# Kernel tuning notes

Hardware: AMD Instinct MI355X
Metric: run time of the kernel (lower is better)

## Reference

```python
import jax, jax.numpy as jnp
import numpy as np

ALPHA = 1.0
BETA = 0.25

B, C, D = 65536, 1024, 64


def setup_inputs() -> dict:
    key = jax.random.key(0)
    k1, k2 = jax.random.split(key)
    z = jax.random.normal(k1, (B, D), dtype=jnp.float32)
    # xavier_normal init for the (C, D) codebook
    std = float(np.sqrt(2.0 / (C + D)))
    codebook = jax.random.normal(k2, (C, D), dtype=jnp.float32) * std
    return {"z": z, "codebook": codebook}


def reference(z, codebook):
    # pairwise squared distances d[b,c] = ||z_b - e_c||^2 via expanded norms
    zn2 = jnp.sum(z * z, axis=1, keepdims=True)          # [B,1]
    wn2 = jnp.sum(codebook * codebook, axis=1)            # [C]
    d = zn2 + wn2 - 2.0 * (z @ codebook.T)               # [B,C]
    # Student-t soft assignment (same value as torch's explicit diff-sum)
    q = jnp.power(1.0 / (1.0 + d / ALPHA), (ALPHA + 1.0) / 2.0)
    q = q / jnp.sum(q, axis=1, keepdims=True)
    # hard assignment: torch code uses argmax over d (faithful to source)
    idx = jnp.argmax(d, axis=1)                          # [B]
    # gather codebook rows (equals one-hot @ codebook)
    z_q = codebook[idx]                                  # [B,D]
    sg = jax.lax.stop_gradient
    loss = BETA * jnp.mean((sg(z_q) - z) ** 2) + jnp.mean((z_q - sg(z)) ** 2)
    # straight-through estimator
    z_q_st = z + sg(z_q - z)
    return q, z_q_st, loss
```

## Files before the change

### kernel.cpp

```cpp
#include <hip/hip_runtime.h>
#include <stdint.h>

#define NB    65536
#define NC    1024
#define ND    64
#define BR    32
#define NW    4


__global__ void vq_prep(const float* __restrict__ cb, float* __restrict__ ws) {
    int c = blockIdx.x * 64 + threadIdx.x;
    float s = 0.f;
    #pragma unroll 8
    for (int k = 0; k < ND; ++k) {
        float v = cb[c * ND + k];
        ws[2048 + k * NC + c] = v;
        s = fmaf(v, v, s);
    }
    ws[64 + c] = s;
}

__device__ inline unsigned long long shfl_xor_u64(unsigned long long v, int m) {
    unsigned lo = (unsigned)v, hi = (unsigned)(v >> 32);
    lo = __shfl_xor(lo, m, 64);
    hi = __shfl_xor(hi, m, 64);
    return ((unsigned long long)hi << 32) | (unsigned long long)lo;
}

__global__ __launch_bounds__(256, 2) void vq_main(
    const float* __restrict__ z, const float* __restrict__ cb,
    const float* __restrict__ ws, float* __restrict__ q_out,
    float* __restrict__ zq_out, float* __restrict__ loss_acc)
{
    const int rb = blockIdx.x * BR;
    const int L  = threadIdx.x;
    const float* __restrict__ zb = z + (size_t)rb * ND;
    const float4* __restrict__ cbT4 = (const float4*)(ws + 2048);
    const float4* __restrict__ wn24 = (const float4*)(ws + 64);

    __shared__ float part[256];
    __shared__ float zn2s[BR];
    __shared__ float sred[NW * BR];
    __shared__ unsigned long long kred[NW * BR];

    {
        const float4* z4 = (const float4*)zb;
        float4 a = z4[L * 2 + 0];
        float4 b = z4[L * 2 + 1];
        part[L] = a.x*a.x + a.y*a.y + a.z*a.z + a.w*a.w
                + b.x*b.x + b.y*b.y + b.z*b.z + b.w*b.w;
    }
    __syncthreads();
    if (L < BR) {
        float s = 0.f;
        #pragma unroll
        for (int j = 0; j < 8; ++j) s += part[L * 8 + j];
        zn2s[L] = s;
    }
    __syncthreads();

    float4 acc[BR];
    #pragma unroll
    for (int r = 0; r < BR; ++r) acc[r] = make_float4(0.f, 0.f, 0.f, 0.f);

    for (int kk = 0; kk < ND; kk += 4) {
        float4 c0 = cbT4[(size_t)(kk + 0) * 256 + L];
        float4 c1 = cbT4[(size_t)(kk + 1) * 256 + L];
        float4 c2 = cbT4[(size_t)(kk + 2) * 256 + L];
        float4 c3 = cbT4[(size_t)(kk + 3) * 256 + L];
        #pragma unroll
        for (int r = 0; r < BR; ++r) {
            float z0 = zb[r * ND + kk + 0];
            float z1 = zb[r * ND + kk + 1];
            float z2 = zb[r * ND + kk + 2];
            float z3 = zb[r * ND + kk + 3];
            float4 a = acc[r];
            a.x = fmaf(z0, c0.x, a.x); a.y = fmaf(z0, c0.y, a.y);
            a.z = fmaf(z0, c0.z, a.z); a.w = fmaf(z0, c0.w, a.w);
            a.x = fmaf(z1, c1.x, a.x); a.y = fmaf(z1, c1.y, a.y);
            a.z = fmaf(z1, c1.z, a.z); a.w = fmaf(z1, c1.w, a.w);
            a.x = fmaf(z2, c2.x, a.x); a.y = fmaf(z2, c2.y, a.y);
            a.z = fmaf(z2, c2.z, a.z); a.w = fmaf(z2, c2.w, a.w);
            a.x = fmaf(z3, c3.x, a.x); a.y = fmaf(z3, c3.y, a.y);
            a.z = fmaf(z3, c3.z, a.z); a.w = fmaf(z3, c3.w, a.w);
            acc[r] = a;
        }
    }

    const int wv = L >> 6, lane = L & 63;
    float4 w4 = wn24[L];
    const int c0i = 4 * L;

    #pragma unroll
    for (int r = 0; r < BR; ++r) {
        float zn2r = zn2s[r];
        float4 a = acc[r];
        float d0 = (zn2r + w4.x) - 2.f * a.x;
        float d1 = (zn2r + w4.y) - 2.f * a.y;
        float d2 = (zn2r + w4.z) - 2.f * a.z;
        float d3 = (zn2r + w4.w) - 2.f * a.w;
        float q0 = __builtin_amdgcn_rcpf(1.f + d0);
        float q1 = __builtin_amdgcn_rcpf(1.f + d1);
        float q2 = __builtin_amdgcn_rcpf(1.f + d2);
        float q3 = __builtin_amdgcn_rcpf(1.f + d3);
        acc[r] = make_float4(q0, q1, q2, q3);
        float ps = ((q0 + q1) + q2) + q3;
        unsigned long long k0 = ((unsigned long long)__float_as_uint(d0) << 32) | (unsigned)(1023 - (c0i + 0));
        unsigned long long k1 = ((unsigned long long)__float_as_uint(d1) << 32) | (unsigned)(1023 - (c0i + 1));
        unsigned long long k2 = ((unsigned long long)__float_as_uint(d2) << 32) | (unsigned)(1023 - (c0i + 2));
        unsigned long long k3 = ((unsigned long long)__float_as_uint(d3) << 32) | (unsigned)(1023 - (c0i + 3));
        unsigned long long ka = k0 > k1 ? k0 : k1;
        unsigned long long kb = k2 > k3 ? k2 : k3;
        unsigned long long key = ka > kb ? ka : kb;
        #pragma unroll
        for (int m = 1; m < 64; m <<= 1) {
            ps += __shfl_xor(ps, m, 64);
            unsigned long long ok = shfl_xor_u64(key, m);
            key = key > ok ? key : ok;
        }
        if (lane == 0) { sred[wv * BR + r] = ps; kred[wv * BR + r] = key; }
    }
    __syncthreads();

    #pragma unroll
    for (int r = 0; r < BR; ++r) {
        float fs = ((sred[0 * BR + r] + sred[1 * BR + r]) + sred[2 * BR + r]) + sred[3 * BR + r];
        float inv = __builtin_amdgcn_rcpf(fs);
        float4 a = acc[r];
        float4 o = make_float4(a.x * inv, a.y * inv, a.z * inv, a.w * inv);
        ((float4*)q_out)[(size_t)(rb + r) * (NC / 4) + L] = o;
    }

    float lsum = 0.f;
    #pragma unroll
    for (int i = 0; i < BR / NW; ++i) {
        int r = wv * (BR / NW) + i;
        unsigned long long ka = kred[0 * BR + r] > kred[1 * BR + r] ? kred[0 * BR + r] : kred[1 * BR + r];
        unsigned long long kb = kred[2 * BR + r] > kred[3 * BR + r] ? kred[2 * BR + r] : kred[3 * BR + r];
        unsigned long long km = ka > kb ? ka : kb;
        int bc = 1023 - (int)(unsigned)(km & 0xffffffffULL);
        float cv = cb[(size_t)bc * ND + lane];
        float zv = z[(size_t)(rb + r) * ND + lane];
        float t = cv - zv;
        zq_out[(size_t)(rb + r) * ND + lane] = zv + t;
        lsum = fmaf(t, t, lsum);
    }
    #pragma unroll
    for (int m = 1; m < 64; m <<= 1) lsum += __shfl_xor(lsum, m, 64);
    if (lane == 0) atomicAdd(loss_acc, lsum);
}

__global__ void vq_fin(const float* __restrict__ ws, float* __restrict__ loss_out) {
    if (threadIdx.x == 0) {
        float m = ws[0] / (float)((size_t)NB * ND);
        loss_out[0] = 0.25f * m + m;
    }
}

extern "C" void kernel_launch(void* const* d_in, const int* in_sizes, int n_in,
                              void* d_out, int out_size, void* d_ws, size_t ws_size,
                              hipStream_t stream) {
    const float* z  = (const float*)d_in[0];
    const float* cb = (const float*)d_in[1];
    float* q_out    = (float*)d_out;
    float* zq_out   = q_out + (size_t)NB * NC;
    float* loss_out = zq_out + (size_t)NB * ND;
    float* ws       = (float*)d_ws;

    hipMemsetAsync(d_ws, 0, 4, stream);
    vq_prep<<<NC / 64, 64, 0, stream>>>(cb, ws);
    vq_main<<<NB / BR, 256, 0, stream>>>(z, cb, ws, q_out, zq_out, ws);
    vq_fin<<<1, 64, 0, stream>>>(ws, loss_out);
}
```

Measured before the change: 419.9 us.

## Halve row tile, stage z rows in LDS, raise occupancy, vectorize prep

The main kernel now processes 16 rows per block instead of 32, stages the z tile in shared memory as float4 instead of reading scalar z values from global memory, and raises the launch-bound occupancy hint from 2 to 4 blocks per CU. The prep kernel is rewritten to use float4 loads with 16 threads per codebook row and a shuffle reduction for the norms. This aims to cut register pressure and improve latency hiding in the memory-bound q write phase. The trade-off is that each codebook column load is reused across half as many rows, doubling codebook traffic from L2.

```diff
diff --git a/kernel.cpp b/kernel.cpp
--- a/kernel.cpp
+++ b/kernel.cpp
@@ -4,20 +4,23 @@
 #define NB    65536
 #define NC    1024
 #define ND    64
-#define BR    32
+#define BR    16
 #define NW    4
 
 
 __global__ void vq_prep(const float* __restrict__ cb, float* __restrict__ ws) {
-    int c = blockIdx.x * 64 + threadIdx.x;
-    float s = 0.f;
-    #pragma unroll 8
-    for (int k = 0; k < ND; ++k) {
-        float v = cb[c * ND + k];
-        ws[2048 + k * NC + c] = v;
-        s = fmaf(v, v, s);
-    }
-    ws[64 + c] = s;
+    int gid = blockIdx.x * 256 + threadIdx.x;
+    int c  = gid >> 4;
+    int kq = gid & 15;
+    float4 v = ((const float4*)cb)[gid];
+    ws[2048 + (4 * kq + 0) * NC + c] = v.x;
+    ws[2048 + (4 * kq + 1) * NC + c] = v.y;
+    ws[2048 + (4 * kq + 2) * NC + c] = v.z;
+    ws[2048 + (4 * kq + 3) * NC + c] = v.w;
+    float s = v.x * v.x + v.y * v.y + v.z * v.z + v.w * v.w;
+    #pragma unroll
+    for (int m = 1; m < 16; m <<= 1) s += __shfl_xor(s, m, 64);
+    if ((threadIdx.x & 15) == 0) ws[64 + c] = s;
 }
 
 __device__ inline unsigned long long shfl_xor_u64(unsigned long long v, int m) {
@@ -27,34 +30,32 @@
     return ((unsigned long long)hi << 32) | (unsigned long long)lo;
 }
 
-__global__ __launch_bounds__(256, 2) void vq_main(
+__global__ __launch_bounds__(256, 4) void vq_main(
     const float* __restrict__ z, const float* __restrict__ cb,
     const float* __restrict__ ws, float* __restrict__ q_out,
     float* __restrict__ zq_out, float* __restrict__ loss_acc)
 {
     const int rb = blockIdx.x * BR;
     const int L  = threadIdx.x;
-    const float* __restrict__ zb = z + (size_t)rb * ND;
     const float4* __restrict__ cbT4 = (const float4*)(ws + 2048);
     const float4* __restrict__ wn24 = (const float4*)(ws + 64);
 
+    __shared__ float4 zs4[BR * 16];
     __shared__ float part[256];
     __shared__ float zn2s[BR];
     __shared__ float sred[NW * BR];
     __shared__ unsigned long long kred[NW * BR];
 
     {
-        const float4* z4 = (const float4*)zb;
-        float4 a = z4[L * 2 + 0];
-        float4 b = z4[L * 2 + 1];
-        part[L] = a.x*a.x + a.y*a.y + a.z*a.z + a.w*a.w
-                + b.x*b.x + b.y*b.y + b.z*b.z + b.w*b.w;
+        float4 v = ((const float4*)z)[(size_t)rb * 16 + L];
+        zs4[L] = v;
+        part[L] = v.x * v.x + v.y * v.y + v.z * v.z + v.w * v.w;
     }
     __syncthreads();
     if (L < BR) {
         float s = 0.f;
         #pragma unroll
-        for (int j = 0; j < 8; ++j) s += part[L * 8 + j];
+        for (int j = 0; j < 16; ++j) s += part[L * 16 + j];
         zn2s[L] = s;
     }
     __syncthreads();
@@ -63,26 +64,24 @@
     #pragma unroll
     for (int r = 0; r < BR; ++r) acc[r] = make_float4(0.f, 0.f, 0.f, 0.f);
 
-    for (int kk = 0; kk < ND; kk += 4) {
-        float4 c0 = cbT4[(size_t)(kk + 0) * 256 + L];
-        float4 c1 = cbT4[(size_t)(kk + 1) * 256 + L];
-        float4 c2 = cbT4[(size_t)(kk + 2) * 256 + L];
-        float4 c3 = cbT4[(size_t)(kk + 3) * 256 + L];
+    #pragma unroll 2
+    for (int kk = 0; kk < 16; ++kk) {
+        float4 c0 = cbT4[(size_t)(4 * kk + 0) * 256 + L];
+        float4 c1 = cbT4[(size_t)(4 * kk + 1) * 256 + L];
+        float4 c2 = cbT4[(size_t)(4 * kk + 2) * 256 + L];
+        float4 c3 = cbT4[(size_t)(4 * kk + 3) * 256 + L];
         #pragma unroll
         for (int r = 0; r < BR; ++r) {
-            float z0 = zb[r * ND + kk + 0];
-            float z1 = zb[r * ND + kk + 1];
-            float z2 = zb[r * ND + kk + 2];
-            float z3 = zb[r * ND + kk + 3];
+            float4 zr = zs4[r * 16 + kk];
             float4 a = acc[r];
-            a.x = fmaf(z0, c0.x, a.x); a.y = fmaf(z0, c0.y, a.y);
-            a.z = fmaf(z0, c0.z, a.z); a.w = fmaf(z0, c0.w, a.w);
-            a.x = fmaf(z1, c1.x, a.x); a.y = fmaf(z1, c1.y, a.y);
-            a.z = fmaf(z1, c1.z, a.z); a.w = fmaf(z1, c1.w, a.w);
-            a.x = fmaf(z2, c2.x, a.x); a.y = fmaf(z2, c2.y, a.y);
-            a.z = fmaf(z2, c2.z, a.z); a.w = fmaf(z2, c2.w, a.w);
-            a.x = fmaf(z3, c3.x, a.x); a.y = fmaf(z3, c3.y, a.y);
-            a.z = fmaf(z3, c3.z, a.z); a.w = fmaf(z3, c3.w, a.w);
+            a.x = fmaf(zr.x, c0.x, a.x); a.y = fmaf(zr.x, c0.y, a.y);
+            a.z = fmaf(zr.x, c0.z, a.z); a.w = fmaf(zr.x, c0.w, a.w);
+            a.x = fmaf(zr.y, c1.x, a.x); a.y = fmaf(zr.y, c1.y, a.y);
+            a.z = fmaf(zr.y, c1.z, a.z); a.w = fmaf(zr.y, c1.w, a.w);
+            a.x = fmaf(zr.z, c2.x, a.x); a.y = fmaf(zr.z, c2.y, a.y);
+            a.z = fmaf(zr.z, c2.z, a.z); a.w = fmaf(zr.z, c2.w, a.w);
+            a.x = fmaf(zr.w, c3.x, a.x); a.y = fmaf(zr.w, c3.y, a.y);
+            a.z = fmaf(zr.w, c3.z, a.z); a.w = fmaf(zr.w, c3.w, a.w);
             acc[r] = a;
         }
     }
@@ -168,7 +167,7 @@
     float* ws       = (float*)d_ws;
 
     hipMemsetAsync(d_ws, 0, 4, stream);
-    vq_prep<<<NC / 64, 64, 0, stream>>>(cb, ws);
+    vq_prep<<<NC * 16 / 256, 256, 0, stream>>>(cb, ws);
     vq_main<<<NB / BR, 256, 0, stream>>>(z, cb, ws, q_out, zq_out, ws);
     vq_fin<<<1, 64, 0, stream>>>(ws, loss_out);
 }
```

Measured after the change: 830.1 us. 1.98x slower.
